# Kernel tuning notes

Measured on AMD Instinct MI355X. Metric: run time of the kernel, lower is better.

The kernel has to match this reference:

```python
import jax, jax.numpy as jnp
import numpy as np

K_PROPOSALS = 16  # Marsaglia-Tsang acceptance rate > 0.95 for alpha > 1/3; P(all 16 rejected) < 1e-20

B, D_IN, H, L = 32768, 1024, 512, 64


def _glorot(key, shape):
    fan_in, fan_out = shape
    return jax.random.normal(key, shape, jnp.float32) * jnp.sqrt(2.0 / (fan_in + fan_out))


def setup_inputs() -> dict:
    key = jax.random.key(0)
    ks = jax.random.split(key, 4)
    return {
        "x": jax.random.normal(ks[0], (B, D_IN), jnp.float32),
        "W0": _glorot(ks[1], (D_IN, H)),
        "b0": jnp.zeros((H,), jnp.float32),
        "W1": _glorot(ks[2], (H, H)),
        "b1": jnp.zeros((H,), jnp.float32),
        "Wl": _glorot(ks[3], (H, L)),
        "bl": jnp.zeros((L,), jnp.float32),
    }


def _marsaglia_tsang_sample(alpha):
    """Vectorized Marsaglia-Tsang gamma(alpha, 1) rejection sampler.
    Draws K_PROPOSALS candidates per element and selects the first accepted one
    (equivalent to the original per-element while-loop, flattened for SIMD)."""
    d = alpha - 1.0 / 3.0                     # [B, L]
    c = 1.0 / jnp.sqrt(9.0 * d)               # [B, L]
    kz, ku = jax.random.split(jax.random.key(1))
    z = jax.random.normal(kz, (K_PROPOSALS,) + alpha.shape, alpha.dtype)   # [K, B, L]
    u = jax.random.uniform(ku, (K_PROPOSALS,) + alpha.shape, alpha.dtype,
                           minval=1e-7, maxval=1.0)                        # [K, B, L]
    v = (1.0 + c * z) ** 3                    # [K, B, L]
    pos = v > 0.0                             # equivalent to z > -1/c (= b1)
    safe_v = jnp.where(pos, v, 1.0)
    # accept iff z > b1 AND log(u) <= b2 (negation of the resampling condition)
    b2 = 0.5 * jnp.square(z) + d - d * safe_v + d * jnp.log(safe_v)
    accept = pos & (jnp.log(u) < b2)          # [K, B, L]
    first = jnp.argmax(accept, axis=0)        # index of first accepted proposal
    samples = d * safe_v                      # [K, B, L]
    return jnp.take_along_axis(samples, first[None], axis=0)[0]  # [B, L]


def reference(x, W0, b0, W1, b1, Wl, bl):
    # dense encoder: two ReLU hidden layers + linear latent head producing alpha
    h = jax.nn.relu(x @ W0 + b0)
    h = jax.nn.relu(h @ W1 + b1)
    # softplus + 0.5 keeps alpha > 1/3 so d > 0 (required by Marsaglia-Tsang)
    alpha = jax.nn.softplus(h @ Wl + bl) + 0.5
    sample = _marsaglia_tsang_sample(alpha)
    return alpha, sample
```

## Files before the change

kernel.cpp:

```cpp
#include <hip/hip_runtime.h>
#include <cstdint>
#include <cstddef>

typedef __attribute__((ext_vector_type(8))) short short8;
typedef __attribute__((ext_vector_type(4))) float floatx4;

constexpr int MDIM = 32768;
constexpr int DIN  = 1024;
constexpr int HDIM = 512;
constexpr int LDIM = 64;
constexpr uint32_t BL = (uint32_t)MDIM * (uint32_t)LDIM;

__host__ __device__ __forceinline__ void tf2x32(uint32_t k0, uint32_t k1,
                                                uint32_t x0, uint32_t x1,
                                                uint32_t& o0, uint32_t& o1) {
  const uint32_t k2 = k0 ^ k1 ^ 0x1BD11BDAu;
  x0 += k0; x1 += k1;
#define TFR(r) { x0 += x1; x1 = (x1 << (r)) | (x1 >> (32 - (r))); x1 ^= x0; }
  TFR(13) TFR(15) TFR(26) TFR(6)
  x0 += k1; x1 += k2 + 1u;
  TFR(17) TFR(29) TFR(16) TFR(24)
  x0 += k2; x1 += k0 + 2u;
  TFR(13) TFR(15) TFR(26) TFR(6)
  x0 += k0; x1 += k1 + 3u;
  TFR(17) TFR(29) TFR(16) TFR(24)
  x0 += k1; x1 += k2 + 4u;
  TFR(13) TFR(15) TFR(26) TFR(6)
  x0 += k2; x1 += k0 + 5u;
#undef TFR
  o0 = x0; o1 = x1;
}

__device__ __forceinline__ uint32_t tf_bits(uint32_t k0, uint32_t k1, uint32_t j) {
  uint32_t o0, o1;
  tf2x32(k0, k1, 0u, j, o0, o1);
  return o0 ^ o1;
}

__device__ __forceinline__ float b2f(unsigned short s) {
  return __uint_as_float((uint32_t)s << 16);
}
__device__ __forceinline__ unsigned short f2b(float f) {
  uint32_t u = __float_as_uint(f);
  u += 0x7fffu + ((u >> 16) & 1u);
  return (unsigned short)(u >> 16);
}
__device__ __forceinline__ void split3(float x, unsigned short& h,
                                       unsigned short& l, unsigned short& l2) {
  h = f2b(x);
  const float r = __fsub_rn(x, b2f(h));
  l = f2b(r);
  const float r2 = __fsub_rn(r, b2f(l));
  l2 = f2b(r2);
}

__device__ __forceinline__ float erfinv_f32(float x) {
  const float xx = __fmul_rn(x, x);
  float w = -log1pf(-xx);
  float p;
  if (w < 5.0f) {
    w = __fadd_rn(w, -2.5f);
    p = 2.81022636e-08f;
    p = __fadd_rn(__fmul_rn(p, w), 3.43273939e-07f);
    p = __fadd_rn(__fmul_rn(p, w), -3.5233877e-06f);
    p = __fadd_rn(__fmul_rn(p, w), -4.39150654e-06f);
    p = __fadd_rn(__fmul_rn(p, w), 0.00021858087f);
    p = __fadd_rn(__fmul_rn(p, w), -0.00125372503f);
    p = __fadd_rn(__fmul_rn(p, w), -0.00417768164f);
    p = __fadd_rn(__fmul_rn(p, w), 0.246640727f);
    p = __fadd_rn(__fmul_rn(p, w), 1.50140941f);
  } else {
    w = __fadd_rn(sqrtf(w), -3.0f);
    p = -0.000200214257f;
    p = __fadd_rn(__fmul_rn(p, w), 0.000100950558f);
    p = __fadd_rn(__fmul_rn(p, w), 0.00134934322f);
    p = __fadd_rn(__fmul_rn(p, w), -0.00367342844f);
    p = __fadd_rn(__fmul_rn(p, w), 0.00573950773f);
    p = __fadd_rn(__fmul_rn(p, w), -0.0076224613f);
    p = __fadd_rn(__fmul_rn(p, w), 0.00943887047f);
    p = __fadd_rn(__fmul_rn(p, w), 1.00167406f);
    p = __fadd_rn(__fmul_rn(p, w), 2.83297682f);
  }
  return __fmul_rn(p, x);
}

#define LO_N  (-0x1.fffffep-1f)
#define DIFF_N (2.0f)
#define SQRT2_F ((float)1.4142135623730951)
#define DIFF_U (0x1.fffffcp-1f)
#define MINV_U (1e-7f)
#define THIRD_F ((float)(1.0 / 3.0))

__device__ float gamma_sample(float alpha, uint32_t e,
                              uint32_t kz0, uint32_t kz1,
                              uint32_t ku0, uint32_t ku1) {
  const float d = __fsub_rn(alpha, THIRD_F);
  const float c = __fdiv_rn(1.0f, sqrtf(__fmul_rn(9.0f, d)));
  float samp0 = 0.0f;
#pragma unroll 1
  for (int k = 0; k < 16; ++k) {
    const uint32_t j = (uint32_t)k * BL + e;
    const uint32_t zb = tf_bits(kz0, kz1, j);
    const uint32_t ub = tf_bits(ku0, ku1, j);
    const float fz = __fsub_rn(__uint_as_float((zb >> 9) | 0x3f800000u), 1.0f);
    float un = __fadd_rn(__fmul_rn(fz, DIFF_N), LO_N);
    un = fmaxf(un, LO_N);
    const float z = __fmul_rn(SQRT2_F, erfinv_f32(un));
    const float fu = __fsub_rn(__uint_as_float((ub >> 9) | 0x3f800000u), 1.0f);
    float uu = __fadd_rn(__fmul_rn(fu, DIFF_U), MINV_U);
    uu = fmaxf(uu, MINV_U);
    const float t1 = __fadd_rn(1.0f, __fmul_rn(c, z));
    const float v = __fmul_rn(t1, __fmul_rn(t1, t1));
    const bool pos = (v > 0.0f);
    const float sv = pos ? v : 1.0f;
    const float b2 = __fadd_rn(
        __fsub_rn(__fadd_rn(__fmul_rn(0.5f, __fmul_rn(z, z)), d),
                  __fmul_rn(d, sv)),
        __fmul_rn(d, logf(sv)));
    const float lu = logf(uu);
    const float s = __fmul_rn(d, sv);
    if (k == 0) samp0 = s;
    if (pos && (lu < b2)) return s;
  }
  return samp0;
}

__global__ __launch_bounds__(256) void split_transpose(
    const float* __restrict__ W, unsigned short* __restrict__ D, int K, int N) {
  __shared__ unsigned short th[32][33], tl[32][33], tl2[32][33];
  const int t = threadIdx.x;
  const int nb = N / 32;
  const int k0 = (blockIdx.x / nb) * 32, n0 = (blockIdx.x % nb) * 32;
#pragma unroll
  for (int i = 0; i < 4; ++i) {
    const int e = i * 256 + t;
    const int kk = e >> 5, nn = e & 31;
    const float x = W[(size_t)(k0 + kk) * N + (n0 + nn)];
    split3(x, th[kk][nn], tl[kk][nn], tl2[kk][nn]);
  }
  __syncthreads();
  const size_t PL = (size_t)N * K;
#pragma unroll
  for (int i = 0; i < 4; ++i) {
    const int e = i * 256 + t;
    const int nn = e >> 5, kk = e & 31;
    const size_t o = (size_t)(n0 + nn) * K + (k0 + kk);
    D[o] = th[kk][nn];
    D[PL + o] = tl[kk][nn];
    D[2 * PL + o] = tl2[kk][nn];
  }
}

template <int K>
__global__ __launch_bounds__(256) void gemm_split_mfma(
    const float* __restrict__ A, const unsigned short* __restrict__ BT,
    const float* __restrict__ bias, float* __restrict__ C) {
  constexpr int N = 512;
  constexpr size_t PL = (size_t)N * K;
  __shared__ unsigned short As[3][128 * 32];
  __shared__ unsigned short Bs[3][128 * 32];
  const int t = threadIdx.x;
  const int lane = t & 63, w = t >> 6;
  const int wm = w >> 1, wn = w & 1;
  const int ln = lane & 15, kq = lane >> 4;
  const int bm = blockIdx.y * 128, bn = blockIdx.x * 128;
  const int rq = kq ^ ((ln >> 1) & 3);
  const int kcs = ((lane & 3) ^ ((lane >> 3) & 3)) * 8;

  floatx4 acc[4][4];
#pragma unroll
  for (int i = 0; i < 4; ++i)
#pragma unroll
    for (int j = 0; j < 4; ++j) acc[i][j] = (floatx4)0.0f;

  for (int k0 = 0; k0 < K; k0 += 32) {
#pragma unroll
    for (int p = 0; p < 3; ++p)
#pragma unroll
      for (int i = 0; i < 2; ++i) {
        const int e = w * 1024 + i * 512 + lane * 8;
        const int n = e >> 5;
        const unsigned short* g = BT + p * PL + (size_t)(bn + n) * K + (k0 + kcs);
        __builtin_amdgcn_global_load_lds(
            (const __attribute__((address_space(1))) unsigned int*)g,
            (__attribute__((address_space(3))) unsigned int*)&Bs[p][w * 1024 + i * 512],
            16, 0, 0);
      }
#pragma unroll
    for (int it = 0; it < 4; ++it) {
      const int e4 = (it * 256 + t) * 4;
      const int m = e4 >> 5, kc = e4 & 31;
      const float4 q = *reinterpret_cast<const float4*>(
          &A[(size_t)(bm + m) * K + (k0 + kc)]);
      ushort4 h, l, l2;
      split3(q.x, h.x, l.x, l2.x);
      split3(q.y, h.y, l.y, l2.y);
      split3(q.z, h.z, l.z, l2.z);
      split3(q.w, h.w, l.w, l2.w);
      const int si = m * 32 + (((kc >> 3) ^ ((m >> 1) & 3)) << 3) + (kc & 7);
      *reinterpret_cast<ushort4*>(&As[0][si]) = h;
      *reinterpret_cast<ushort4*>(&As[1][si]) = l;
      *reinterpret_cast<ushort4*>(&As[2][si]) = l2;
    }
    __syncthreads();
    short8 af[3][4], bf[3][4];
#pragma unroll
    for (int mi = 0; mi < 4; ++mi)
#pragma unroll
      for (int p = 0; p < 3; ++p)
        af[p][mi] = *reinterpret_cast<const short8*>(
            &As[p][(wm * 64 + mi * 16 + ln) * 32 + rq * 8]);
#pragma unroll
    for (int ni = 0; ni < 4; ++ni)
#pragma unroll
      for (int p = 0; p < 3; ++p)
        bf[p][ni] = *reinterpret_cast<const short8*>(
            &Bs[p][(wn * 64 + ni * 16 + ln) * 32 + rq * 8]);
#pragma unroll
    for (int mi = 0; mi < 4; ++mi)
#pragma unroll
      for (int ni = 0; ni < 4; ++ni) {
        floatx4 a = acc[mi][ni];
        a = __builtin_amdgcn_mfma_f32_16x16x32_bf16(af[0][mi], bf[0][ni], a, 0, 0, 0);
        a = __builtin_amdgcn_mfma_f32_16x16x32_bf16(af[0][mi], bf[1][ni], a, 0, 0, 0);
        a = __builtin_amdgcn_mfma_f32_16x16x32_bf16(af[1][mi], bf[0][ni], a, 0, 0, 0);
        a = __builtin_amdgcn_mfma_f32_16x16x32_bf16(af[1][mi], bf[1][ni], a, 0, 0, 0);
        a = __builtin_amdgcn_mfma_f32_16x16x32_bf16(af[0][mi], bf[2][ni], a, 0, 0, 0);
        a = __builtin_amdgcn_mfma_f32_16x16x32_bf16(af[2][mi], bf[0][ni], a, 0, 0, 0);
        acc[mi][ni] = a;
      }
    __syncthreads();
  }
#pragma unroll
  for (int ni = 0; ni < 4; ++ni) {
    const int n = bn + wn * 64 + ni * 16 + ln;
    const float bb = bias[n];
#pragma unroll
    for (int mi = 0; mi < 4; ++mi)
#pragma unroll
      for (int r = 0; r < 4; ++r) {
        const int m = bm + wm * 64 + mi * 16 + kq * 4 + r;
        C[(size_t)m * N + n] = fmaxf(__fadd_rn(acc[mi][ni][r], bb), 0.0f);
      }
  }
}

__global__ __launch_bounds__(256) void gemm3_sampler(
    const float* __restrict__ A, const unsigned short* __restrict__ BT,
    const float* __restrict__ bl, float* __restrict__ out,
    uint32_t kz0, uint32_t kz1, uint32_t ku0, uint32_t ku1) {
  constexpr int K = 512, N = 64;
  constexpr size_t PL = (size_t)N * K;
  __shared__ unsigned short As[3][64 * 32];
  __shared__ unsigned short Bs[3][64 * 32];
  const int t = threadIdx.x;
  const int lane = t & 63, w = t >> 6;
  const int ln = lane & 15, kq = lane >> 4;
  const int bm = blockIdx.x * 64;
  const int rq = kq ^ ((ln >> 1) & 3);
  const int kcs = ((lane & 3) ^ ((lane >> 3) & 3)) * 8;

  floatx4 acc[4];
#pragma unroll
  for (int j = 0; j < 4; ++j) acc[j] = (floatx4)0.0f;

  for (int k0 = 0; k0 < K; k0 += 32) {
#pragma unroll
    for (int p = 0; p < 3; ++p) {
      const int n = w * 16 + (lane >> 2);
      const unsigned short* g = BT + p * PL + (size_t)n * K + (k0 + kcs);
      __builtin_amdgcn_global_load_lds(
          (const __attribute__((address_space(1))) unsigned int*)g,
          (__attribute__((address_space(3))) unsigned int*)&Bs[p][w * 512],
          16, 0, 0);
    }
#pragma unroll
    for (int it = 0; it < 2; ++it) {
      const int e4 = (it * 256 + t) * 4;
      const int m = e4 >> 5, kc = e4 & 31;
      const float4 q = *reinterpret_cast<const float4*>(
          &A[(size_t)(bm + m) * K + (k0 + kc)]);
      ushort4 h, l, l2;
      split3(q.x, h.x, l.x, l2.x);
      split3(q.y, h.y, l.y, l2.y);
      split3(q.z, h.z, l.z, l2.z);
      split3(q.w, h.w, l.w, l2.w);
      const int si = m * 32 + (((kc >> 3) ^ ((m >> 1) & 3)) << 3) + (kc & 7);
      *reinterpret_cast<ushort4*>(&As[0][si]) = h;
      *reinterpret_cast<ushort4*>(&As[1][si]) = l;
      *reinterpret_cast<ushort4*>(&As[2][si]) = l2;
    }
    __syncthreads();
    short8 af[3];
#pragma unroll
    for (int p = 0; p < 3; ++p)
      af[p] = *reinterpret_cast<const short8*>(
          &As[p][(w * 16 + ln) * 32 + rq * 8]);
#pragma unroll
    for (int ni = 0; ni < 4; ++ni) {
      const short8 b0 = *reinterpret_cast<const short8*>(
          &Bs[0][(ni * 16 + ln) * 32 + rq * 8]);
      const short8 b1 = *reinterpret_cast<const short8*>(
          &Bs[1][(ni * 16 + ln) * 32 + rq * 8]);
      const short8 b2 = *reinterpret_cast<const short8*>(
          &Bs[2][(ni * 16 + ln) * 32 + rq * 8]);
      floatx4 a = acc[ni];
      a = __builtin_amdgcn_mfma_f32_16x16x32_bf16(af[0], b0, a, 0, 0, 0);
      a = __builtin_amdgcn_mfma_f32_16x16x32_bf16(af[0], b1, a, 0, 0, 0);
      a = __builtin_amdgcn_mfma_f32_16x16x32_bf16(af[1], b0, a, 0, 0, 0);
      a = __builtin_amdgcn_mfma_f32_16x16x32_bf16(af[1], b1, a, 0, 0, 0);
      a = __builtin_amdgcn_mfma_f32_16x16x32_bf16(af[0], b2, a, 0, 0, 0);
      a = __builtin_amdgcn_mfma_f32_16x16x32_bf16(af[2], b0, a, 0, 0, 0);
      acc[ni] = a;
    }
    __syncthreads();
  }
#pragma unroll
  for (int ni = 0; ni < 4; ++ni) {
    const int n = ni * 16 + ln;
    const float bb = bl[n];
#pragma unroll
    for (int r = 0; r < 4; ++r) {
      const int m = bm + w * 16 + kq * 4 + r;
      const float x = __fadd_rn(acc[ni][r], bb);
      const float sp = __fadd_rn(fmaxf(x, 0.0f), log1pf(expf(-fabsf(x))));
      const float alpha = __fadd_rn(sp, 0.5f);
      const uint32_t e = (uint32_t)m * 64u + (uint32_t)n;
      const float s = gamma_sample(alpha, e, kz0, kz1, ku0, ku1);
      out[(size_t)m * 64 + n] = alpha;
      out[(size_t)BL + (size_t)m * 64 + n] = s;
    }
  }
}

extern "C" void kernel_launch(void* const* d_in, const int* in_sizes, int n_in,
                              void* d_out, int out_size, void* d_ws, size_t ws_size,
                              hipStream_t stream) {
  (void)in_sizes; (void)n_in; (void)out_size; (void)ws_size;
  const float* x  = (const float*)d_in[0];
  const float* W0 = (const float*)d_in[1];
  const float* b0 = (const float*)d_in[2];
  const float* W1 = (const float*)d_in[3];
  const float* b1 = (const float*)d_in[4];
  const float* Wl = (const float*)d_in[5];
  const float* bl = (const float*)d_in[6];
  float* h1 = (float*)d_ws;
  float* h2 = h1 + (size_t)MDIM * HDIM;
  float* out = (float*)d_out;

  unsigned short* W0T = (unsigned short*)out;
  unsigned short* W1T = (unsigned short*)(out + BL);
  unsigned short* WlT = (unsigned short*)d_ws;

  uint32_t kz0, kz1, ku0, ku1;
  tf2x32(0u, 1u, 0u, 0u, kz0, kz1);
  tf2x32(0u, 1u, 0u, 1u, ku0, ku1);

  split_transpose<<<dim3((DIN / 32) * (HDIM / 32)), 256, 0, stream>>>(
      W0, W0T, DIN, HDIM);
  split_transpose<<<dim3((HDIM / 32) * (HDIM / 32)), 256, 0, stream>>>(
      W1, W1T, HDIM, HDIM);

  dim3 g12(HDIM / 128, MDIM / 128);
  gemm_split_mfma<DIN><<<g12, 256, 0, stream>>>(x, W0T, b0, h1);
  gemm_split_mfma<HDIM><<<g12, 256, 0, stream>>>(h1, W1T, b1, h2);

  split_transpose<<<dim3((HDIM / 32) * (LDIM / 32)), 256, 0, stream>>>(
      Wl, WlT, HDIM, LDIM);

  gemm3_sampler<<<dim3(MDIM / 64), 256, 0, stream>>>(h2, WlT, bl, out,
                                                     kz0, kz1, ku0, ku1);
}
```

Before: 502.2 us.

## Software-pipeline GEMM K-loops with double-buffered B and register-prefetched A

Both GEMM kernels now prefetch the next K-slice while computing the current one. B tiles go into a double-buffered LDS region via async global-to-LDS loads, and A is held in registers and split/stored after the compute barrier. The main GEMM also remaps block IDs so that consecutive blocks share rows of A for L2 locality. The sampler GEMM is widened to 512 threads with a 2x4 wave split so more waves share the epilogue sampling work. The costs are extra LDS, higher register pressure from the prefetched values, and an extra barrier per step.

```diff
diff --git a/kernel.cpp b/kernel.cpp
--- a/kernel.cpp
+++ b/kernel.cpp
@@ -156,16 +156,21 @@
     const float* __restrict__ A, const unsigned short* __restrict__ BT,
     const float* __restrict__ bias, float* __restrict__ C) {
   constexpr int N = 512;
+  constexpr int NS = K / 32;
   constexpr size_t PL = (size_t)N * K;
   __shared__ unsigned short As[3][128 * 32];
-  __shared__ unsigned short Bs[3][128 * 32];
+  __shared__ unsigned short Bs[2][3][128 * 32];
   const int t = threadIdx.x;
   const int lane = t & 63, w = t >> 6;
   const int wm = w >> 1, wn = w & 1;
   const int ln = lane & 15, kq = lane >> 4;
-  const int bm = blockIdx.y * 128, bn = blockIdx.x * 128;
+  const int bid = blockIdx.y * gridDim.x + blockIdx.x;
+  const int L = (bid & 7) * 128 + (bid >> 3);
+  const int bm = (L >> 2) * 128, bn = (L & 3) * 128;
   const int rq = kq ^ ((ln >> 1) & 3);
   const int kcs = ((lane & 3) ^ ((lane >> 3) & 3)) * 8;
+  const int arow = t >> 3, acol = (t * 4) & 31;
+  const int swz = ((((acol >> 3) ^ ((arow >> 1) & 3)) << 3) | (acol & 7));
 
   floatx4 acc[4][4];
 #pragma unroll
@@ -173,64 +178,123 @@
 #pragma unroll
     for (int j = 0; j < 4; ++j) acc[i][j] = (floatx4)0.0f;
 
-  for (int k0 = 0; k0 < K; k0 += 32) {
+  {
+    float4 q0 = *reinterpret_cast<const float4*>(
+        &A[(size_t)(bm + 0 * 32 + arow) * K + acol]);
+    float4 q1 = *reinterpret_cast<const float4*>(
+        &A[(size_t)(bm + 1 * 32 + arow) * K + acol]);
+    float4 q2 = *reinterpret_cast<const float4*>(
+        &A[(size_t)(bm + 2 * 32 + arow) * K + acol]);
+    float4 q3 = *reinterpret_cast<const float4*>(
+        &A[(size_t)(bm + 3 * 32 + arow) * K + acol]);
 #pragma unroll
     for (int p = 0; p < 3; ++p)
 #pragma unroll
       for (int i = 0; i < 2; ++i) {
-        const int e = w * 1024 + i * 512 + lane * 8;
-        const int n = e >> 5;
-        const unsigned short* g = BT + p * PL + (size_t)(bn + n) * K + (k0 + kcs);
+        const int n = w * 32 + i * 16 + (lane >> 2);
+        const unsigned short* g = BT + p * PL + (size_t)(bn + n) * K + kcs;
         __builtin_amdgcn_global_load_lds(
             (const __attribute__((address_space(1))) unsigned int*)g,
-            (__attribute__((address_space(3))) unsigned int*)&Bs[p][w * 1024 + i * 512],
+            (__attribute__((address_space(3))) unsigned int*)
+                &Bs[0][p][w * 1024 + i * 512],
             16, 0, 0);
       }
 #pragma unroll
     for (int it = 0; it < 4; ++it) {
-      const int e4 = (it * 256 + t) * 4;
-      const int m = e4 >> 5, kc = e4 & 31;
-      const float4 q = *reinterpret_cast<const float4*>(
-          &A[(size_t)(bm + m) * K + (k0 + kc)]);
+      const float4 q = (it == 0) ? q0 : (it == 1) ? q1 : (it == 2) ? q2 : q3;
       ushort4 h, l, l2;
       split3(q.x, h.x, l.x, l2.x);
       split3(q.y, h.y, l.y, l2.y);
       split3(q.z, h.z, l.z, l2.z);
       split3(q.w, h.w, l.w, l2.w);
-      const int si = m * 32 + (((kc >> 3) ^ ((m >> 1) & 3)) << 3) + (kc & 7);
+      const int si = (it * 32 + arow) * 32 + swz;
       *reinterpret_cast<ushort4*>(&As[0][si]) = h;
       *reinterpret_cast<ushort4*>(&As[1][si]) = l;
       *reinterpret_cast<ushort4*>(&As[2][si]) = l2;
     }
     __syncthreads();
-    short8 af[3][4], bf[3][4];
-#pragma unroll
-    for (int mi = 0; mi < 4; ++mi)
-#pragma unroll
-      for (int p = 0; p < 3; ++p)
-        af[p][mi] = *reinterpret_cast<const short8*>(
-            &As[p][(wm * 64 + mi * 16 + ln) * 32 + rq * 8]);
-#pragma unroll
-    for (int ni = 0; ni < 4; ++ni)
-#pragma unroll
-      for (int p = 0; p < 3; ++p)
-        bf[p][ni] = *reinterpret_cast<const short8*>(
-            &Bs[p][(wn * 64 + ni * 16 + ln) * 32 + rq * 8]);
-#pragma unroll
-    for (int mi = 0; mi < 4; ++mi)
-#pragma unroll
-      for (int ni = 0; ni < 4; ++ni) {
-        floatx4 a = acc[mi][ni];
-        a = __builtin_amdgcn_mfma_f32_16x16x32_bf16(af[0][mi], bf[0][ni], a, 0, 0, 0);
-        a = __builtin_amdgcn_mfma_f32_16x16x32_bf16(af[0][mi], bf[1][ni], a, 0, 0, 0);
-        a = __builtin_amdgcn_mfma_f32_16x16x32_bf16(af[1][mi], bf[0][ni], a, 0, 0, 0);
-        a = __builtin_amdgcn_mfma_f32_16x16x32_bf16(af[1][mi], bf[1][ni], a, 0, 0, 0);
-        a = __builtin_amdgcn_mfma_f32_16x16x32_bf16(af[0][mi], bf[2][ni], a, 0, 0, 0);
-        a = __builtin_amdgcn_mfma_f32_16x16x32_bf16(af[2][mi], bf[0][ni], a, 0, 0, 0);
-        acc[mi][ni] = a;
-      }
-    __syncthreads();
-  }
+  }
+
+#define GEMM_STEP(SREAD, BRD, BWR)                                            \
+  {                                                                           \
+    const int snext = (SREAD) + 1;                                            \
+    const bool pf = (snext < NS);                                             \
+    float4 q0, q1, q2, q3;                                                    \
+    if (pf) {                                                                 \
+      const int kk = snext * 32;                                              \
+      q0 = *reinterpret_cast<const float4*>(                                  \
+          &A[(size_t)(bm + 0 * 32 + arow) * K + kk + acol]);                  \
+      q1 = *reinterpret_cast<const float4*>(                                  \
+          &A[(size_t)(bm + 1 * 32 + arow) * K + kk + acol]);                  \
+      q2 = *reinterpret_cast<const float4*>(                                  \
+          &A[(size_t)(bm + 2 * 32 + arow) * K + kk + acol]);                  \
+      q3 = *reinterpret_cast<const float4*>(                                  \
+          &A[(size_t)(bm + 3 * 32 + arow) * K + kk + acol]);                  \
+      _Pragma("unroll")                                                       \
+      for (int p = 0; p < 3; ++p)                                             \
+        _Pragma("unroll")                                                     \
+        for (int i = 0; i < 2; ++i) {                                         \
+          const int n = w * 32 + i * 16 + (lane >> 2);                        \
+          const unsigned short* g =                                           \
+              BT + p * PL + (size_t)(bn + n) * K + (kk + kcs);                \
+          __builtin_amdgcn_global_load_lds(                                   \
+              (const __attribute__((address_space(1))) unsigned int*)g,       \
+              (__attribute__((address_space(3))) unsigned int*)               \
+                  &(BWR)[p][w * 1024 + i * 512],                              \
+              16, 0, 0);                                                      \
+        }                                                                     \
+    }                                                                         \
+    short8 af[3][4], bf[3][4];                                                \
+    _Pragma("unroll")                                                         \
+    for (int mi = 0; mi < 4; ++mi)                                            \
+      _Pragma("unroll")                                                       \
+      for (int p = 0; p < 3; ++p)                                             \
+        af[p][mi] = *reinterpret_cast<const short8*>(                         \
+            &As[p][(wm * 64 + mi * 16 + ln) * 32 + rq * 8]);                  \
+    _Pragma("unroll")                                                         \
+    for (int ni = 0; ni < 4; ++ni)                                            \
+      _Pragma("unroll")                                                       \
+      for (int p = 0; p < 3; ++p)                                             \
+        bf[p][ni] = *reinterpret_cast<const short8*>(                         \
+            &(BRD)[p][(wn * 64 + ni * 16 + ln) * 32 + rq * 8]);               \
+    _Pragma("unroll")                                                         \
+    for (int mi = 0; mi < 4; ++mi)                                            \
+      _Pragma("unroll")                                                       \
+      for (int ni = 0; ni < 4; ++ni) {                                        \
+        floatx4 a = acc[mi][ni];                                              \
+        a = __builtin_amdgcn_mfma_f32_16x16x32_bf16(af[0][mi], bf[0][ni], a, 0, 0, 0); \
+        a = __builtin_amdgcn_mfma_f32_16x16x32_bf16(af[0][mi], bf[1][ni], a, 0, 0, 0); \
+        a = __builtin_amdgcn_mfma_f32_16x16x32_bf16(af[1][mi], bf[0][ni], a, 0, 0, 0); \
+        a = __builtin_amdgcn_mfma_f32_16x16x32_bf16(af[1][mi], bf[1][ni], a, 0, 0, 0); \
+        a = __builtin_amdgcn_mfma_f32_16x16x32_bf16(af[0][mi], bf[2][ni], a, 0, 0, 0); \
+        a = __builtin_amdgcn_mfma_f32_16x16x32_bf16(af[2][mi], bf[0][ni], a, 0, 0, 0); \
+        acc[mi][ni] = a;                                                      \
+      }                                                                       \
+    __syncthreads();                                                          \
+    if (pf) {                                                                 \
+      _Pragma("unroll")                                                       \
+      for (int it = 0; it < 4; ++it) {                                        \
+        const float4 q = (it == 0) ? q0 : (it == 1) ? q1 : (it == 2) ? q2 : q3; \
+        ushort4 h, l, l2;                                                     \
+        split3(q.x, h.x, l.x, l2.x);                                          \
+        split3(q.y, h.y, l.y, l2.y);                                          \
+        split3(q.z, h.z, l.z, l2.z);                                          \
+        split3(q.w, h.w, l.w, l2.w);                                          \
+        const int si = (it * 32 + arow) * 32 + swz;                           \
+        *reinterpret_cast<ushort4*>(&As[0][si]) = h;                          \
+        *reinterpret_cast<ushort4*>(&As[1][si]) = l;                          \
+        *reinterpret_cast<ushort4*>(&As[2][si]) = l2;                         \
+      }                                                                       \
+    }                                                                         \
+    __syncthreads();                                                          \
+  }
+
+  for (int s = 0; s < NS; s += 2) {
+    GEMM_STEP(s, Bs[0], Bs[1]);
+    GEMM_STEP(s + 1, Bs[1], Bs[0]);
+  }
+#undef GEMM_STEP
+
 #pragma unroll
   for (int ni = 0; ni < 4; ++ni) {
     const int n = bn + wn * 64 + ni * 16 + ln;
@@ -245,84 +309,125 @@
   }
 }
 
-__global__ __launch_bounds__(256) void gemm3_sampler(
+__global__ __launch_bounds__(512) void gemm3_sampler(
     const float* __restrict__ A, const unsigned short* __restrict__ BT,
     const float* __restrict__ bl, float* __restrict__ out,
     uint32_t kz0, uint32_t kz1, uint32_t ku0, uint32_t ku1) {
-  constexpr int K = 512, N = 64;
+  constexpr int K = 512, N = 64, NS = K / 32;
   constexpr size_t PL = (size_t)N * K;
   __shared__ unsigned short As[3][64 * 32];
-  __shared__ unsigned short Bs[3][64 * 32];
+  __shared__ unsigned short Bs[2][3][64 * 32];
   const int t = threadIdx.x;
   const int lane = t & 63, w = t >> 6;
+  const int wm = w >> 1, wn = w & 1;
   const int ln = lane & 15, kq = lane >> 4;
   const int bm = blockIdx.x * 64;
   const int rq = kq ^ ((ln >> 1) & 3);
   const int kcs = ((lane & 3) ^ ((lane >> 3) & 3)) * 8;
-
-  floatx4 acc[4];
-#pragma unroll
-  for (int j = 0; j < 4; ++j) acc[j] = (floatx4)0.0f;
-
-  for (int k0 = 0; k0 < K; k0 += 32) {
-#pragma unroll
-    for (int p = 0; p < 3; ++p) {
-      const int n = w * 16 + (lane >> 2);
-      const unsigned short* g = BT + p * PL + (size_t)n * K + (k0 + kcs);
+  const int arow = t >> 3, acol = (t * 4) & 31;
+  const int swz = ((((acol >> 3) ^ ((arow >> 1) & 3)) << 3) | (acol & 7));
+
+  floatx4 acc[2];
+  acc[0] = (floatx4)0.0f;
+  acc[1] = (floatx4)0.0f;
+
+  {
+    const float4 q = *reinterpret_cast<const float4*>(
+        &A[(size_t)(bm + arow) * K + acol]);
+    for (int s2 = w; s2 < 12; s2 += 8) {
+      const int p = s2 >> 2, half = s2 & 3;
+      const int n = half * 16 + (lane >> 2);
+      const unsigned short* g = BT + p * PL + (size_t)n * K + kcs;
       __builtin_amdgcn_global_load_lds(
           (const __attribute__((address_space(1))) unsigned int*)g,
-          (__attribute__((address_space(3))) unsigned int*)&Bs[p][w * 512],
+          (__attribute__((address_space(3))) unsigned int*)
+              &Bs[0][p][half * 512],
           16, 0, 0);
     }
-#pragma unroll
-    for (int it = 0; it < 2; ++it) {
-      const int e4 = (it * 256 + t) * 4;
-      const int m = e4 >> 5, kc = e4 & 31;
-      const float4 q = *reinterpret_cast<const float4*>(
-          &A[(size_t)(bm + m) * K + (k0 + kc)]);
-      ushort4 h, l, l2;
-      split3(q.x, h.x, l.x, l2.x);
-      split3(q.y, h.y, l.y, l2.y);
-      split3(q.z, h.z, l.z, l2.z);
-      split3(q.w, h.w, l.w, l2.w);
-      const int si = m * 32 + (((kc >> 3) ^ ((m >> 1) & 3)) << 3) + (kc & 7);
-      *reinterpret_cast<ushort4*>(&As[0][si]) = h;
-      *reinterpret_cast<ushort4*>(&As[1][si]) = l;
-      *reinterpret_cast<ushort4*>(&As[2][si]) = l2;
-    }
+    ushort4 h, l, l2;
+    split3(q.x, h.x, l.x, l2.x);
+    split3(q.y, h.y, l.y, l2.y);
+    split3(q.z, h.z, l.z, l2.z);
+    split3(q.w, h.w, l.w, l2.w);
+    const int si = arow * 32 + swz;
+    *reinterpret_cast<ushort4*>(&As[0][si]) = h;
+    *reinterpret_cast<ushort4*>(&As[1][si]) = l;
+    *reinterpret_cast<ushort4*>(&As[2][si]) = l2;
     __syncthreads();
-    short8 af[3];
-#pragma unroll
-    for (int p = 0; p < 3; ++p)
-      af[p] = *reinterpret_cast<const short8*>(
-          &As[p][(w * 16 + ln) * 32 + rq * 8]);
-#pragma unroll
-    for (int ni = 0; ni < 4; ++ni) {
-      const short8 b0 = *reinterpret_cast<const short8*>(
-          &Bs[0][(ni * 16 + ln) * 32 + rq * 8]);
-      const short8 b1 = *reinterpret_cast<const short8*>(
-          &Bs[1][(ni * 16 + ln) * 32 + rq * 8]);
-      const short8 b2 = *reinterpret_cast<const short8*>(
-          &Bs[2][(ni * 16 + ln) * 32 + rq * 8]);
-      floatx4 a = acc[ni];
-      a = __builtin_amdgcn_mfma_f32_16x16x32_bf16(af[0], b0, a, 0, 0, 0);
-      a = __builtin_amdgcn_mfma_f32_16x16x32_bf16(af[0], b1, a, 0, 0, 0);
-      a = __builtin_amdgcn_mfma_f32_16x16x32_bf16(af[1], b0, a, 0, 0, 0);
-      a = __builtin_amdgcn_mfma_f32_16x16x32_bf16(af[1], b1, a, 0, 0, 0);
-      a = __builtin_amdgcn_mfma_f32_16x16x32_bf16(af[0], b2, a, 0, 0, 0);
-      a = __builtin_amdgcn_mfma_f32_16x16x32_bf16(af[2], b0, a, 0, 0, 0);
-      acc[ni] = a;
-    }
-    __syncthreads();
-  }
-#pragma unroll
-  for (int ni = 0; ni < 4; ++ni) {
-    const int n = ni * 16 + ln;
+  }
+
+#define G3_STEP(SREAD, BRD, BWR)                                              \
+  {                                                                           \
+    const int snext = (SREAD) + 1;                                            \
+    const bool pf = (snext < NS);                                             \
+    float4 q;                                                                 \
+    if (pf) {                                                                 \
+      const int kk = snext * 32;                                              \
+      q = *reinterpret_cast<const float4*>(                                   \
+          &A[(size_t)(bm + arow) * K + kk + acol]);                           \
+      for (int s2 = w; s2 < 12; s2 += 8) {                                    \
+        const int p = s2 >> 2, half = s2 & 3;                                 \
+        const int n = half * 16 + (lane >> 2);                                \
+        const unsigned short* g =                                             \
+            BT + p * PL + (size_t)n * K + (kk + kcs);                         \
+        __builtin_amdgcn_global_load_lds(                                     \
+            (const __attribute__((address_space(1))) unsigned int*)g,         \
+            (__attribute__((address_space(3))) unsigned int*)                 \
+                &(BWR)[p][half * 512],                                        \
+            16, 0, 0);                                                        \
+      }                                                                       \
+    }                                                                         \
+    short8 af[3], bf[3][2];                                                   \
+    _Pragma("unroll")                                                         \
+    for (int p = 0; p < 3; ++p)                                               \
+      af[p] = *reinterpret_cast<const short8*>(                               \
+          &As[p][(wm * 16 + ln) * 32 + rq * 8]);                              \
+    _Pragma("unroll")                                                         \
+    for (int j = 0; j < 2; ++j)                                               \
+      _Pragma("unroll")                                                       \
+      for (int p = 0; p < 3; ++p)                                             \
+        bf[p][j] = *reinterpret_cast<const short8*>(                          \
+            &(BRD)[p][(wn * 32 + j * 16 + ln) * 32 + rq * 8]);                \
+    _Pragma("unroll")                                                         \
+    for (int j = 0; j < 2; ++j) {                                             \
+      floatx4 a = acc[j];                                                     \
+      a = __builtin_amdgcn_mfma_f32_16x16x32_bf16(af[0], bf[0][j], a, 0, 0, 0); \
+      a = __builtin_amdgcn_mfma_f32_16x16x32_bf16(af[0], bf[1][j], a, 0, 0, 0); \
+      a = __builtin_amdgcn_mfma_f32_16x16x32_bf16(af[1], bf[0][j], a, 0, 0, 0); \
+      a = __builtin_amdgcn_mfma_f32_16x16x32_bf16(af[1], bf[1][j], a, 0, 0, 0); \
+      a = __builtin_amdgcn_mfma_f32_16x16x32_bf16(af[0], bf[2][j], a, 0, 0, 0); \
+      a = __builtin_amdgcn_mfma_f32_16x16x32_bf16(af[2], bf[0][j], a, 0, 0, 0); \
+      acc[j] = a;                                                             \
+    }                                                                         \
+    __syncthreads();                                                          \
+    if (pf) {                                                                 \
+      ushort4 h, l, l2;                                                       \
+      split3(q.x, h.x, l.x, l2.x);                                            \
+      split3(q.y, h.y, l.y, l2.y);                                            \
+      split3(q.z, h.z, l.z, l2.z);                                            \
+      split3(q.w, h.w, l.w, l2.w);                                            \
+      const int si = arow * 32 + swz;                                         \
+      *reinterpret_cast<ushort4*>(&As[0][si]) = h;                            \
+      *reinterpret_cast<ushort4*>(&As[1][si]) = l;                            \
+      *reinterpret_cast<ushort4*>(&As[2][si]) = l2;                           \
+    }                                                                         \
+    __syncthreads();                                                          \
+  }
+
+  for (int s = 0; s < NS; s += 2) {
+    G3_STEP(s, Bs[0], Bs[1]);
+    G3_STEP(s + 1, Bs[1], Bs[0]);
+  }
+#undef G3_STEP
+
+#pragma unroll
+  for (int j = 0; j < 2; ++j) {
+    const int n = wn * 32 + j * 16 + ln;
     const float bb = bl[n];
 #pragma unroll
     for (int r = 0; r < 4; ++r) {
-      const int m = bm + w * 16 + kq * 4 + r;
-      const float x = __fadd_rn(acc[ni][r], bb);
+      const int m = bm + wm * 16 + kq * 4 + r;
+      const float x = __fadd_rn(acc[j][r], bb);
       const float sp = __fadd_rn(fmaxf(x, 0.0f), log1pf(expf(-fabsf(x))));
       const float alpha = __fadd_rn(sp, 0.5f);
       const uint32_t e = (uint32_t)m * 64u + (uint32_t)n;
@@ -340,8 +445,8 @@
   const float* x  = (const float*)d_in[0];
   const float* W0 = (const float*)d_in[1];
   const float* b0 = (const float*)d_in[2];
+  const float* b1 = (const float*)d_in[4];
   const float* W1 = (const float*)d_in[3];
-  const float* b1 = (const float*)d_in[4];
   const float* Wl = (const float*)d_in[5];
   const float* bl = (const float*)d_in[6];
   float* h1 = (float*)d_ws;
@@ -368,6 +473,6 @@
   split_transpose<<<dim3((HDIM / 32) * (LDIM / 32)), 256, 0, stream>>>(
       Wl, WlT, HDIM, LDIM);
 
-  gemm3_sampler<<<dim3(MDIM / 64), 256, 0, stream>>>(h2, WlT, bl, out,
+  gemm3_sampler<<<dim3(MDIM / 64), 512, 0, stream>>>(h2, WlT, bl, out,
                                                      kz0, kz1, ku0, ku1);
 }
```

New measurement: 523.0 us. 1.04x slower.

## Double-buffer weight tiles and load A fragments directly into registers

Applied to the files above, without the earlier changes.

Both GEMM kernels drop the shared-memory A tile. Each wave now loads its fp32 A fragment straight from global memory and splits it into three bf16 parts in registers. The B (weight) tiles are double-buffered in LDS, so the next k-slice is fetched asynchronously while the current one is multiplied, with one barrier per step instead of two. The hidden-layer GEMM also remaps block IDs so neighbouring blocks share A rows for cache locality and requests 3 blocks per CU. The sampler kernel moves to 512 threads, each wave covering half the N columns. The cost is redundant global A loads across waves that share rows, plus higher register pressure.

```diff
diff --git a/kernel.cpp b/kernel.cpp
--- a/kernel.cpp
+++ b/kernel.cpp
@@ -152,18 +152,20 @@
 }
 
 template <int K>
-__global__ __launch_bounds__(256) void gemm_split_mfma(
+__global__ __launch_bounds__(256, 3) void gemm_split_mfma(
     const float* __restrict__ A, const unsigned short* __restrict__ BT,
     const float* __restrict__ bias, float* __restrict__ C) {
   constexpr int N = 512;
+  constexpr int NS = K / 32;
   constexpr size_t PL = (size_t)N * K;
-  __shared__ unsigned short As[3][128 * 32];
-  __shared__ unsigned short Bs[3][128 * 32];
+  __shared__ unsigned short Bs[2][3][128 * 32];
   const int t = threadIdx.x;
   const int lane = t & 63, w = t >> 6;
   const int wm = w >> 1, wn = w & 1;
   const int ln = lane & 15, kq = lane >> 4;
-  const int bm = blockIdx.y * 128, bn = blockIdx.x * 128;
+  const int bid = blockIdx.y * gridDim.x + blockIdx.x;
+  const int L = (bid & 7) * 128 + (bid >> 3);
+  const int bm = (L >> 2) * 128, bn = (L & 3) * 128;
   const int rq = kq ^ ((ln >> 1) & 3);
   const int kcs = ((lane & 3) ^ ((lane >> 3) & 3)) * 8;
 
@@ -173,64 +175,79 @@
 #pragma unroll
     for (int j = 0; j < 4; ++j) acc[i][j] = (floatx4)0.0f;
 
-  for (int k0 = 0; k0 < K; k0 += 32) {
-#pragma unroll
-    for (int p = 0; p < 3; ++p)
-#pragma unroll
-      for (int i = 0; i < 2; ++i) {
-        const int e = w * 1024 + i * 512 + lane * 8;
-        const int n = e >> 5;
-        const unsigned short* g = BT + p * PL + (size_t)(bn + n) * K + (k0 + kcs);
-        __builtin_amdgcn_global_load_lds(
-            (const __attribute__((address_space(1))) unsigned int*)g,
-            (__attribute__((address_space(3))) unsigned int*)&Bs[p][w * 1024 + i * 512],
-            16, 0, 0);
-      }
-#pragma unroll
-    for (int it = 0; it < 4; ++it) {
-      const int e4 = (it * 256 + t) * 4;
-      const int m = e4 >> 5, kc = e4 & 31;
-      const float4 q = *reinterpret_cast<const float4*>(
-          &A[(size_t)(bm + m) * K + (k0 + kc)]);
-      ushort4 h, l, l2;
-      split3(q.x, h.x, l.x, l2.x);
-      split3(q.y, h.y, l.y, l2.y);
-      split3(q.z, h.z, l.z, l2.z);
-      split3(q.w, h.w, l.w, l2.w);
-      const int si = m * 32 + (((kc >> 3) ^ ((m >> 1) & 3)) << 3) + (kc & 7);
-      *reinterpret_cast<ushort4*>(&As[0][si]) = h;
-      *reinterpret_cast<ushort4*>(&As[1][si]) = l;
-      *reinterpret_cast<ushort4*>(&As[2][si]) = l2;
+#define STAGE_B(KK, BUF)                                                      \
+  _Pragma("unroll")                                                           \
+  for (int p = 0; p < 3; ++p)                                                 \
+    _Pragma("unroll")                                                         \
+    for (int i = 0; i < 2; ++i) {                                             \
+      const int n = w * 32 + i * 16 + (lane >> 2);                            \
+      const unsigned short* g = BT + p * PL + (size_t)(bn + n) * K + ((KK) + kcs); \
+      __builtin_amdgcn_global_load_lds(                                       \
+          (const __attribute__((address_space(1))) unsigned int*)g,           \
+          (__attribute__((address_space(3))) unsigned int*)                   \
+              &(BUF)[p][w * 1024 + i * 512],                                  \
+          16, 0, 0);                                                          \
     }
-    __syncthreads();
-    short8 af[3][4], bf[3][4];
-#pragma unroll
-    for (int mi = 0; mi < 4; ++mi)
-#pragma unroll
-      for (int p = 0; p < 3; ++p)
-        af[p][mi] = *reinterpret_cast<const short8*>(
-            &As[p][(wm * 64 + mi * 16 + ln) * 32 + rq * 8]);
-#pragma unroll
-    for (int ni = 0; ni < 4; ++ni)
-#pragma unroll
-      for (int p = 0; p < 3; ++p)
-        bf[p][ni] = *reinterpret_cast<const short8*>(
-            &Bs[p][(wn * 64 + ni * 16 + ln) * 32 + rq * 8]);
-#pragma unroll
-    for (int mi = 0; mi < 4; ++mi)
-#pragma unroll
-      for (int ni = 0; ni < 4; ++ni) {
-        floatx4 a = acc[mi][ni];
-        a = __builtin_amdgcn_mfma_f32_16x16x32_bf16(af[0][mi], bf[0][ni], a, 0, 0, 0);
-        a = __builtin_amdgcn_mfma_f32_16x16x32_bf16(af[0][mi], bf[1][ni], a, 0, 0, 0);
-        a = __builtin_amdgcn_mfma_f32_16x16x32_bf16(af[1][mi], bf[0][ni], a, 0, 0, 0);
-        a = __builtin_amdgcn_mfma_f32_16x16x32_bf16(af[1][mi], bf[1][ni], a, 0, 0, 0);
-        a = __builtin_amdgcn_mfma_f32_16x16x32_bf16(af[0][mi], bf[2][ni], a, 0, 0, 0);
-        a = __builtin_amdgcn_mfma_f32_16x16x32_bf16(af[2][mi], bf[0][ni], a, 0, 0, 0);
-        acc[mi][ni] = a;
-      }
-    __syncthreads();
-  }
+
+  STAGE_B(0, Bs[0])
+  __syncthreads();
+
+#define GEMM_STEP(S, BRD, BWR)                                                \
+  {                                                                           \
+    const int k0 = (S) * 32;                                                  \
+    if ((S) + 1 < NS) { STAGE_B(k0 + 32, BWR) }                               \
+                    \
+    float4 qa[4][2];                                                          \
+    _Pragma("unroll")                                                         \
+    for (int mi = 0; mi < 4; ++mi) {                                          \
+      const float* ap =                                                       \
+          &A[(size_t)(bm + wm * 64 + mi * 16 + ln) * K + k0 + kq * 8];        \
+      qa[mi][0] = *reinterpret_cast<const float4*>(ap);                       \
+      qa[mi][1] = *reinterpret_cast<const float4*>(ap + 4);                   \
+    }                                                                         \
+    short8 af0[4], af1[4], af2[4];                                            \
+    _Pragma("unroll")                                                         \
+    for (int mi = 0; mi < 4; ++mi) {                                          \
+      float v[8];                                                             \
+      *reinterpret_cast<float4*>(&v[0]) = qa[mi][0];                          \
+      *reinterpret_cast<float4*>(&v[4]) = qa[mi][1];                          \
+      short8 h8, l8, l28;                                                     \
+      _Pragma("unroll")                                                       \
+      for (int j = 0; j < 8; ++j) {                                           \
+        unsigned short hh, ll, ll2;                                           \
+        split3(v[j], hh, ll, ll2);                                            \
+        h8[j] = (short)hh; l8[j] = (short)ll; l28[j] = (short)ll2;            \
+      }                                                                       \
+      af0[mi] = h8; af1[mi] = l8; af2[mi] = l28;                              \
+    }                                                                         \
+    _Pragma("unroll")                                                         \
+    for (int ni = 0; ni < 4; ++ni) {                                          \
+      const int bo = (wn * 64 + ni * 16 + ln) * 32 + rq * 8;                  \
+      const short8 b0 = *reinterpret_cast<const short8*>(&(BRD)[0][bo]);      \
+      const short8 b1 = *reinterpret_cast<const short8*>(&(BRD)[1][bo]);      \
+      const short8 b2 = *reinterpret_cast<const short8*>(&(BRD)[2][bo]);      \
+      _Pragma("unroll")                                                       \
+      for (int mi = 0; mi < 4; ++mi) {                                        \
+        floatx4 a = acc[mi][ni];                                              \
+        a = __builtin_amdgcn_mfma_f32_16x16x32_bf16(af0[mi], b0, a, 0, 0, 0); \
+        a = __builtin_amdgcn_mfma_f32_16x16x32_bf16(af0[mi], b1, a, 0, 0, 0); \
+        a = __builtin_amdgcn_mfma_f32_16x16x32_bf16(af1[mi], b0, a, 0, 0, 0); \
+        a = __builtin_amdgcn_mfma_f32_16x16x32_bf16(af1[mi], b1, a, 0, 0, 0); \
+        a = __builtin_amdgcn_mfma_f32_16x16x32_bf16(af0[mi], b2, a, 0, 0, 0); \
+        a = __builtin_amdgcn_mfma_f32_16x16x32_bf16(af2[mi], b0, a, 0, 0, 0); \
+        acc[mi][ni] = a;                                                      \
+      }                                                                       \
+    }                                                                         \
+    __syncthreads();                                                          \
+  }
+
+  for (int s = 0; s < NS; s += 2) {
+    GEMM_STEP(s, Bs[0], Bs[1])
+    GEMM_STEP(s + 1, Bs[1], Bs[0])
+  }
+#undef GEMM_STEP
+#undef STAGE_B
+
 #pragma unroll
   for (int ni = 0; ni < 4; ++ni) {
     const int n = bn + wn * 64 + ni * 16 + ln;
@@ -245,84 +262,90 @@
   }
 }
 
-__global__ __launch_bounds__(256) void gemm3_sampler(
+__global__ __launch_bounds__(512) void gemm3_sampler(
     const float* __restrict__ A, const unsigned short* __restrict__ BT,
     const float* __restrict__ bl, float* __restrict__ out,
     uint32_t kz0, uint32_t kz1, uint32_t ku0, uint32_t ku1) {
-  constexpr int K = 512, N = 64;
+  constexpr int K = 512, N = 64, NS = K / 32;
   constexpr size_t PL = (size_t)N * K;
-  __shared__ unsigned short As[3][64 * 32];
-  __shared__ unsigned short Bs[3][64 * 32];
+  __shared__ unsigned short Bs[2][3][64 * 32];
   const int t = threadIdx.x;
   const int lane = t & 63, w = t >> 6;
+  const int wm = w >> 1, wn = w & 1;
   const int ln = lane & 15, kq = lane >> 4;
   const int bm = blockIdx.x * 64;
   const int rq = kq ^ ((ln >> 1) & 3);
   const int kcs = ((lane & 3) ^ ((lane >> 3) & 3)) * 8;
 
-  floatx4 acc[4];
-#pragma unroll
-  for (int j = 0; j < 4; ++j) acc[j] = (floatx4)0.0f;
-
-  for (int k0 = 0; k0 < K; k0 += 32) {
-#pragma unroll
-    for (int p = 0; p < 3; ++p) {
-      const int n = w * 16 + (lane >> 2);
-      const unsigned short* g = BT + p * PL + (size_t)n * K + (k0 + kcs);
-      __builtin_amdgcn_global_load_lds(
-          (const __attribute__((address_space(1))) unsigned int*)g,
-          (__attribute__((address_space(3))) unsigned int*)&Bs[p][w * 512],
-          16, 0, 0);
-    }
-#pragma unroll
-    for (int it = 0; it < 2; ++it) {
-      const int e4 = (it * 256 + t) * 4;
-      const int m = e4 >> 5, kc = e4 & 31;
-      const float4 q = *reinterpret_cast<const float4*>(
-          &A[(size_t)(bm + m) * K + (k0 + kc)]);
-      ushort4 h, l, l2;
-      split3(q.x, h.x, l.x, l2.x);
-      split3(q.y, h.y, l.y, l2.y);
-      split3(q.z, h.z, l.z, l2.z);
-      split3(q.w, h.w, l.w, l2.w);
-      const int si = m * 32 + (((kc >> 3) ^ ((m >> 1) & 3)) << 3) + (kc & 7);
-      *reinterpret_cast<ushort4*>(&As[0][si]) = h;
-      *reinterpret_cast<ushort4*>(&As[1][si]) = l;
-      *reinterpret_cast<ushort4*>(&As[2][si]) = l2;
-    }
-    __syncthreads();
-    short8 af[3];
-#pragma unroll
-    for (int p = 0; p < 3; ++p)
-      af[p] = *reinterpret_cast<const short8*>(
-          &As[p][(w * 16 + ln) * 32 + rq * 8]);
-#pragma unroll
-    for (int ni = 0; ni < 4; ++ni) {
-      const short8 b0 = *reinterpret_cast<const short8*>(
-          &Bs[0][(ni * 16 + ln) * 32 + rq * 8]);
-      const short8 b1 = *reinterpret_cast<const short8*>(
-          &Bs[1][(ni * 16 + ln) * 32 + rq * 8]);
-      const short8 b2 = *reinterpret_cast<const short8*>(
-          &Bs[2][(ni * 16 + ln) * 32 + rq * 8]);
-      floatx4 a = acc[ni];
-      a = __builtin_amdgcn_mfma_f32_16x16x32_bf16(af[0], b0, a, 0, 0, 0);
-      a = __builtin_amdgcn_mfma_f32_16x16x32_bf16(af[0], b1, a, 0, 0, 0);
-      a = __builtin_amdgcn_mfma_f32_16x16x32_bf16(af[1], b0, a, 0, 0, 0);
-      a = __builtin_amdgcn_mfma_f32_16x16x32_bf16(af[1], b1, a, 0, 0, 0);
-      a = __builtin_amdgcn_mfma_f32_16x16x32_bf16(af[0], b2, a, 0, 0, 0);
-      a = __builtin_amdgcn_mfma_f32_16x16x32_bf16(af[2], b0, a, 0, 0, 0);
-      acc[ni] = a;
-    }
-    __syncthreads();
-  }
-#pragma unroll
-  for (int ni = 0; ni < 4; ++ni) {
-    const int n = ni * 16 + ln;
+  floatx4 acc[2];
+  acc[0] = (floatx4)0.0f;
+  acc[1] = (floatx4)0.0f;
+
+#define STAGE_B3(KK, BUF)                                                     \
+  for (int s2 = w; s2 < 12; s2 += 8) {                                        \
+    const int p = s2 >> 2, half = s2 & 3;                                     \
+    const int n = half * 16 + (lane >> 2);                                    \
+    const unsigned short* g = BT + p * PL + (size_t)n * K + ((KK) + kcs);     \
+    __builtin_amdgcn_global_load_lds(                                         \
+        (const __attribute__((address_space(1))) unsigned int*)g,             \
+        (__attribute__((address_space(3))) unsigned int*)                     \
+            &(BUF)[p][half * 512],                                            \
+        16, 0, 0);                                                            \
+  }
+
+  STAGE_B3(0, Bs[0])
+  __syncthreads();
+
+#define G3_STEP(S, BRD, BWR)                                                  \
+  {                                                                           \
+    const int k0 = (S) * 32;                                                  \
+    if ((S) + 1 < NS) { STAGE_B3(k0 + 32, BWR) }                              \
+    const float* ap = &A[(size_t)(bm + wm * 16 + ln) * K + k0 + kq * 8];      \
+    const float4 qa0 = *reinterpret_cast<const float4*>(ap);                  \
+    const float4 qa1 = *reinterpret_cast<const float4*>(ap + 4);              \
+    float v[8];                                                               \
+    *reinterpret_cast<float4*>(&v[0]) = qa0;                                  \
+    *reinterpret_cast<float4*>(&v[4]) = qa1;                                  \
+    short8 af0, af1, af2;                                                     \
+    _Pragma("unroll")                                                         \
+    for (int j = 0; j < 8; ++j) {                                             \
+      unsigned short hh, ll, ll2;                                             \
+      split3(v[j], hh, ll, ll2);                                              \
+      af0[j] = (short)hh; af1[j] = (short)ll; af2[j] = (short)ll2;            \
+    }                                                                         \
+    _Pragma("unroll")                                                         \
+    for (int j = 0; j < 2; ++j) {                                             \
+      const int bo = (wn * 32 + j * 16 + ln) * 32 + rq * 8;                   \
+      const short8 b0 = *reinterpret_cast<const short8*>(&(BRD)[0][bo]);      \
+      const short8 b1 = *reinterpret_cast<const short8*>(&(BRD)[1][bo]);      \
+      const short8 b2 = *reinterpret_cast<const short8*>(&(BRD)[2][bo]);      \
+      floatx4 a = acc[j];                                                     \
+      a = __builtin_amdgcn_mfma_f32_16x16x32_bf16(af0, b0, a, 0, 0, 0);       \
+      a = __builtin_amdgcn_mfma_f32_16x16x32_bf16(af0, b1, a, 0, 0, 0);       \
+      a = __builtin_amdgcn_mfma_f32_16x16x32_bf16(af1, b0, a, 0, 0, 0);       \
+      a = __builtin_amdgcn_mfma_f32_16x16x32_bf16(af1, b1, a, 0, 0, 0);       \
+      a = __builtin_amdgcn_mfma_f32_16x16x32_bf16(af0, b2, a, 0, 0, 0);       \
+      a = __builtin_amdgcn_mfma_f32_16x16x32_bf16(af2, b0, a, 0, 0, 0);       \
+      acc[j] = a;                                                             \
+    }                                                                         \
+    __syncthreads();                                                          \
+  }
+
+  for (int s = 0; s < NS; s += 2) {
+    G3_STEP(s, Bs[0], Bs[1])
+    G3_STEP(s + 1, Bs[1], Bs[0])
+  }
+#undef G3_STEP
+#undef STAGE_B3
+
+#pragma unroll
+  for (int j = 0; j < 2; ++j) {
+    const int n = wn * 32 + j * 16 + ln;
     const float bb = bl[n];
 #pragma unroll
     for (int r = 0; r < 4; ++r) {
-      const int m = bm + w * 16 + kq * 4 + r;
-      const float x = __fadd_rn(acc[ni][r], bb);
+      const int m = bm + wm * 16 + kq * 4 + r;
+      const float x = __fadd_rn(acc[j][r], bb);
       const float sp = __fadd_rn(fmaxf(x, 0.0f), log1pf(expf(-fabsf(x))));
       const float alpha = __fadd_rn(sp, 0.5f);
       const uint32_t e = (uint32_t)m * 64u + (uint32_t)n;
@@ -368,6 +391,6 @@
   split_transpose<<<dim3((HDIM / 32) * (LDIM / 32)), 256, 0, stream>>>(
       Wl, WlT, HDIM, LDIM);
 
-  gemm3_sampler<<<dim3(MDIM / 64), 256, 0, stream>>>(h2, WlT, bl, out,
+  gemm3_sampler<<<dim3(MDIM / 64), 512, 0, stream>>>(h2, WlT, bl, out,
                                                      kz0, kz1, ku0, ku1);
 }
```

Result: slower. 891.4 us (+77.5%).
